# Kernel optimization log

Hardware: AMD Instinct MI355X
Metric: run time of the kernel (lower is better)

## Reference

```python
import jax, jax.numpy as jnp
import numpy as np

B, T, E, H = 2, 2048, 2048, 16
D = E // H


def setup_inputs() -> dict:
    key = jax.random.key(0)
    ks = jax.random.split(key, 5)
    s = 0.02
    return {
        "x": jax.random.normal(ks[0], (B, T, E), jnp.float32),
        "Wq": jax.random.normal(ks[1], (E, E), jnp.float32) * s,
        "Wk": jax.random.normal(ks[2], (E, E), jnp.float32) * s,
        "Wv": jax.random.normal(ks[3], (E, E), jnp.float32) * s,
        "Wp": jax.random.normal(ks[4], (E, E), jnp.float32) * s,
        "bp": jnp.zeros((E,), jnp.float32),
    }


def reference(x, Wq, Wk, Wv, Wp, bp):
    b, t, e = x.shape
    h, d = H, E // H
    # torch Linear: y = x @ W.T (no bias for qkv)
    Q = (x @ Wq.T).reshape(b, h, t, d)  # faithful: view without transpose
    K = (x @ Wk.T).reshape(b, h, t, d)
    V = (x @ Wv.T).reshape(b, h, t, d)
    scores = jnp.einsum("bhqd,bhkd->bhqk", Q, K)
    causal = jnp.triu(jnp.ones((t, t), bool), k=1)  # True above diagonal
    scores = jnp.where(causal, -jnp.inf, scores)
    weights = jax.nn.softmax(scores / jnp.sqrt(jnp.float32(d)), axis=-1)
    # dropout p=0.0 (eval) -> identity
    ctx = jnp.einsum("bhqk,bhkd->bhqd", weights, V)  # (b,h,t,d)
    ctx = ctx.transpose(0, 2, 1, 3).reshape(b, t, e)
    return ctx @ Wp.T + bp
```

## Files before the change

### kernel.cpp

```cpp
#include <hip/hip_runtime.h>

#define SEQ   2048
#define EMB   2048
#define NHEAD 16
#define HDIM  128
#define ROWSM 4096

typedef float  f32x4   __attribute__((ext_vector_type(4)));
typedef float  f32x16  __attribute__((ext_vector_type(16)));
typedef __bf16 bf16x8  __attribute__((ext_vector_type(8)));

__device__ __forceinline__ unsigned short f2bf(float f) {
  union { float f; unsigned int u; } v; v.f = f;
  return (unsigned short)((v.u + 0x7fffu + ((v.u >> 16) & 1u)) >> 16);
}
__device__ __forceinline__ unsigned int pk2(float a, float b) {
  return (unsigned int)f2bf(a) | ((unsigned int)f2bf(b) << 16);
}

__device__ __forceinline__ void gload16(const void* g, void* l) {
  __builtin_amdgcn_global_load_lds(
      (__attribute__((address_space(1))) const unsigned int*)g,
      (__attribute__((address_space(3))) unsigned int*)l,
      16, 0, 0);
}

__global__ void cvt_bf16(const float* __restrict__ in,
                         unsigned short* __restrict__ out, int n4) {
  int i = blockIdx.x * 256 + threadIdx.x;
  if (i >= n4) return;
  float4 v = ((const float4*)in)[i];
  ushort4 o;
  o.x = f2bf(v.x); o.y = f2bf(v.y); o.z = f2bf(v.z); o.w = f2bf(v.w);
  ((ushort4*)out)[i] = o;
}

__global__ void cvt_bf16_3(const float* __restrict__ i0, const float* __restrict__ i1,
                           const float* __restrict__ i2, unsigned short* __restrict__ o0,
                           unsigned short* __restrict__ o1, unsigned short* __restrict__ o2,
                           int n4) {
  const float* in = (blockIdx.z == 0) ? i0 : (blockIdx.z == 1) ? i1 : i2;
  unsigned short* out = (blockIdx.z == 0) ? o0 : (blockIdx.z == 1) ? o1 : o2;
  int i = blockIdx.x * 256 + threadIdx.x;
  if (i >= n4) return;
  float4 v = ((const float4*)in)[i];
  ushort4 o;
  o.x = f2bf(v.x); o.y = f2bf(v.y); o.z = f2bf(v.z); o.w = f2bf(v.w);
  ((ushort4*)out)[i] = o;
}

__global__ __launch_bounds__(256, 2) void gemm_qkv(
    const unsigned short* __restrict__ A,
    const unsigned short* __restrict__ B0, const unsigned short* __restrict__ B1,
    const unsigned short* __restrict__ B2, unsigned short* __restrict__ Cbase) {
  __shared__ __align__(16) unsigned short As[128 * 64];
  __shared__ __align__(16) unsigned short Bs[128 * 64];
  const unsigned short* Bm = (blockIdx.z == 0) ? B0 : (blockIdx.z == 1) ? B1 : B2;
  unsigned short* C = Cbase + (size_t)blockIdx.z * ROWSM * EMB;

  const int tid  = threadIdx.x;
  const int lane = tid & 63;
  const int w    = tid >> 6;
  const int m0 = blockIdx.y * 128;
  const int n0 = blockIdx.x * 128;
  const int wm = (w >> 1) * 64;
  const int wn = (w & 1) * 64;
  const int lg = lane >> 4;
  const int lc = lane & 15;

  f32x4 acc[4][4] = {};
  const int srow = lane >> 3;
  const int scol = (lane & 7) * 8;

  for (int k0 = 0; k0 < EMB; k0 += 64) {
    if (k0) __syncthreads();
#pragma unroll
    for (int ii = 0; ii < 4; ++ii) {
      int i = w * 4 + ii;
      int r = i * 8 + srow;
      gload16(A  + (size_t)(m0 + r) * EMB + k0 + scol, (char*)As + i * 1024);
      gload16(Bm + (size_t)(n0 + r) * EMB + k0 + scol, (char*)Bs + i * 1024);
    }
    __syncthreads();
#pragma unroll
    for (int kk = 0; kk < 2; ++kk) {
      const int co = kk * 32 + lg * 8;
      bf16x8 a[4], b[4];
#pragma unroll
      for (int i = 0; i < 4; ++i)
        a[i] = *(const bf16x8*)(As + (wm + i * 16 + lc) * 64 + co);
#pragma unroll
      for (int j = 0; j < 4; ++j)
        b[j] = *(const bf16x8*)(Bs + (wn + j * 16 + lc) * 64 + co);
#pragma unroll
      for (int i = 0; i < 4; ++i)
#pragma unroll
        for (int j = 0; j < 4; ++j)
          acc[i][j] = __builtin_amdgcn_mfma_f32_16x16x32_bf16(a[i], b[j], acc[i][j], 0, 0, 0);
    }
  }

  const int rb = lg * 4;
#pragma unroll
  for (int i = 0; i < 4; ++i)
#pragma unroll
    for (int j = 0; j < 4; ++j) {
      int col = n0 + wn + j * 16 + lc;
#pragma unroll
      for (int r = 0; r < 4; ++r) {
        int row = m0 + wm + i * 16 + rb + r;
        C[(size_t)row * EMB + col] = f2bf(acc[i][j][r]);
      }
    }
}

__global__ __launch_bounds__(256, 2) void gemm_p(
    const unsigned short* __restrict__ A, const unsigned short* __restrict__ B,
    float* __restrict__ Cout, const float* __restrict__ bias) {
  __shared__ __align__(16) unsigned short As[128 * 64];
  __shared__ __align__(16) unsigned short Bs[128 * 64];
  const int tid  = threadIdx.x;
  const int lane = tid & 63;
  const int w    = tid >> 6;
  const int m0 = blockIdx.y * 128;
  const int n0 = blockIdx.x * 128;
  const int wm = (w >> 1) * 64;
  const int wn = (w & 1) * 64;
  const int lg = lane >> 4;
  const int lc = lane & 15;

  f32x4 acc[4][4] = {};
  const int srow = lane >> 3;
  const int scol = (lane & 7) * 8;

  for (int k0 = 0; k0 < EMB; k0 += 64) {
    if (k0) __syncthreads();
#pragma unroll
    for (int ii = 0; ii < 4; ++ii) {
      int i = w * 4 + ii;
      int r = i * 8 + srow;
      gload16(A + (size_t)(m0 + r) * EMB + k0 + scol, (char*)As + i * 1024);
      gload16(B + (size_t)(n0 + r) * EMB + k0 + scol, (char*)Bs + i * 1024);
    }
    __syncthreads();
#pragma unroll
    for (int kk = 0; kk < 2; ++kk) {
      const int co = kk * 32 + lg * 8;
      bf16x8 a[4], b[4];
#pragma unroll
      for (int i = 0; i < 4; ++i)
        a[i] = *(const bf16x8*)(As + (wm + i * 16 + lc) * 64 + co);
#pragma unroll
      for (int j = 0; j < 4; ++j)
        b[j] = *(const bf16x8*)(Bs + (wn + j * 16 + lc) * 64 + co);
#pragma unroll
      for (int i = 0; i < 4; ++i)
#pragma unroll
        for (int j = 0; j < 4; ++j)
          acc[i][j] = __builtin_amdgcn_mfma_f32_16x16x32_bf16(a[i], b[j], acc[i][j], 0, 0, 0);
    }
  }

  const int rb = lg * 4;
#pragma unroll
  for (int i = 0; i < 4; ++i)
#pragma unroll
    for (int j = 0; j < 4; ++j) {
      int col = n0 + wn + j * 16 + lc;
#pragma unroll
      for (int r = 0; r < 4; ++r) {
        int row = m0 + wm + i * 16 + rb + r;
        Cout[(size_t)row * EMB + col] = acc[i][j][r] + bias[col];
      }
    }
}

__global__ __launch_bounds__(256, 2) void attn_causal(
    const unsigned short* __restrict__ Pq, const unsigned short* __restrict__ Pk,
    const unsigned short* __restrict__ Pv, unsigned short* __restrict__ ctx) {
  __shared__ __align__(16) unsigned short Ks[128 * 128];
  __shared__ __align__(16) unsigned short Vt[128 * 128];

  const int tid  = threadIdx.x;
  const int lane = tid & 63;
  const int w    = tid >> 6;
  const int ql   = lane & 31;
  const int hi   = lane >> 5;
  const int lg   = lane >> 4;
  const int lc   = lane & 15;

  const int bid = blockIdx.x;
  const int xcd = bid & 7;
  const int jj_ = bid >> 3;
  const int hh  = jj_ >> 4;
  const int bh  = xcd * 4 + hh;
  const int b   = bh >> 4;
  const int h   = bh & 15;
  const int qtr = jj_ & 15;
  const int qt  = (hh >= 2) ? (15 - qtr) : qtr;
  const int q0 = qt * 128;
  const int qw = q0 + w * 32;
  const int qg = qw + ql;

  const size_t hoff = (size_t)bh * SEQ * HDIM;
  const unsigned short* Q  = Pq + hoff;
  const unsigned short* Kh = Pk + hoff;
  const unsigned short* Vh = Pv + hoff;

  bf16x8 bq[8];
#pragma unroll
  for (int d8 = 0; d8 < 8; ++d8)
    bq[d8] = *(const bf16x8*)(Q + (size_t)qg * HDIM + d8 * 16 + hi * 8);

  const float NEG = -3.0e38f;
  f32x16 o[4];
#pragma unroll
  for (int dt = 0; dt < 4; ++dt)
#pragma unroll
    for (int r = 0; r < 16; ++r) o[dt][r] = 0.f;
  float m_r = NEG, l_r = 0.f;

  const float Cs   = 0.12753123161692858f;
  const float TDEF = 62.7f;

  const int nt128 = qt + 1;
  for (int tt = 0; tt < nt128; ++tt) {
    const int kv0 = tt * 128;
    if (tt) __syncthreads();
#pragma unroll
    for (int ii = 0; ii < 8; ++ii) {
      int i = w * 8 + ii;
      int r = i * 4 + lg;
      int sd = lc ^ (r & 7);
      gload16(Kh + (size_t)(kv0 + r) * HDIM + sd * 8, (char*)Ks + i * 1024);
    }
#pragma unroll 1
    for (int hv = 0; hv < 2; ++hv) {
      uint4 vr[4];
      const unsigned short* Vs = Vh + (size_t)(kv0 + hv * 64) * HDIM;
#pragma unroll
      for (int uu = 0; uu < 2; ++uu) {
        int u = tid + uu * 256;
        int kp = u >> 4, dg = u & 15;
        int k = kp * 2, d0 = dg * 8;
        vr[uu * 2]     = *(const uint4*)(Vs + (size_t)k * HDIM + d0);
        vr[uu * 2 + 1] = *(const uint4*)(Vs + (size_t)(k + 1) * HDIM + d0);
      }
#pragma unroll
      for (int uu = 0; uu < 2; ++uu) {
        int u = tid + uu * 256;
        int kp = u >> 4, dg = u & 15;
        int k = kp * 2, d0 = dg * 8;
        const unsigned short* e0 = (const unsigned short*)&vr[uu * 2];
        const unsigned short* e1 = (const unsigned short*)&vr[uu * 2 + 1];
#pragma unroll
        for (int jj = 0; jj < 8; ++jj) {
          int d = d0 + jj;
          int slot = ((hv << 3) | (k >> 3)) ^ jj ^ (dg & 7);
          int byteoff = d * 256 + (slot << 4) + (k & 7) * 2;
          *(unsigned int*)((char*)Vt + byteoff) =
              (unsigned int)e0[jj] | ((unsigned int)e1[jj] << 16);
        }
      }
    }
    __syncthreads();

#pragma unroll 1
    for (int hf = 0; hf < 2; ++hf) {
      const int kv0h = kv0 + hf * 64;
      if (kv0h > qw + 31) continue;
      const bool s1on = (kv0h + 32 <= qw + 31);
      const bool diag = (kv0h + 63 > qw);
      const char* ksb = (const char*)Ks + hf * 64 * 256;

      f32x16 c0, c1;
#pragma unroll
      for (int r = 0; r < 16; ++r) { c0[r] = 0.f; c1[r] = s1on ? 0.f : NEG; }
      __builtin_amdgcn_s_setprio(1);
#pragma unroll
      for (int d8 = 0; d8 < 8; ++d8) {
        bf16x8 ak = *(const bf16x8*)(ksb + ql * 256 +
                                     (((d8 * 2 + hi) ^ (ql & 7)) << 4));
        c0 = __builtin_amdgcn_mfma_f32_32x32x16_bf16(ak, bq[d8], c0, 0, 0, 0);
      }
      if (s1on) {
#pragma unroll
        for (int d8 = 0; d8 < 8; ++d8) {
          bf16x8 ak = *(const bf16x8*)(ksb + (32 + ql) * 256 +
                                       (((d8 * 2 + hi) ^ (ql & 7)) << 4));
          c1 = __builtin_amdgcn_mfma_f32_32x32x16_bf16(ak, bq[d8], c1, 0, 0, 0);
        }
      }
      __builtin_amdgcn_s_setprio(0);

      if (diag) {
#pragma unroll
        for (int r = 0; r < 16; ++r) {
          int kvl = (r & 3) + 8 * (r >> 2) + 4 * hi;
          if (kv0h + kvl > qg) c0[r] = NEG;
          if (s1on && kv0h + 32 + kvl > qg) c1[r] = NEG;
        }
      }
      float rm = c0[0];
#pragma unroll
      for (int r = 1; r < 16; ++r) rm = fmaxf(rm, c0[r]);
#pragma unroll
      for (int r = 0; r < 16; ++r) rm = fmaxf(rm, c1[r]);
      rm = fmaxf(rm, __shfl_xor(rm, 32));

      if (__any(rm > m_r + TDEF)) {
        float mnew = fmaxf(m_r, rm);
        float alpha = exp2f((m_r - mnew) * Cs);
        m_r = mnew;
        l_r *= alpha;
#pragma unroll
        for (int r = 0; r < 16; ++r) {
          float ar = __shfl(alpha, (r & 3) + 8 * (r >> 2) + 4 * hi);
#pragma unroll
          for (int dt = 0; dt < 4; ++dt) o[dt][r] *= ar;
        }
      }
#pragma unroll
      for (int r = 0; r < 16; ++r) {
        c0[r] = exp2f((c0[r] - m_r) * Cs);
        c1[r] = exp2f((c1[r] - m_r) * Cs);
      }
      float ps = 0.f;
#pragma unroll
      for (int r = 0; r < 16; ++r) ps += c0[r] + c1[r];
      ps += __shfl_xor(ps, 32);
      l_r += ps;

      bf16x8 pa[4];
#pragma unroll
      for (int t4 = 0; t4 < 4; ++t4) {
        const f32x16& cc = (t4 < 2) ? c0 : c1;
        const int rA = (t4 & 1) * 8;
        unsigned int pkL0 = pk2(cc[rA + 0], cc[rA + 1]);
        unsigned int pkL1 = pk2(cc[rA + 2], cc[rA + 3]);
        unsigned int pkH0 = pk2(cc[rA + 4], cc[rA + 5]);
        unsigned int pkH1 = pk2(cc[rA + 6], cc[rA + 7]);
        unsigned int give0 = hi ? pkL0 : pkH0;
        unsigned int give1 = hi ? pkL1 : pkH1;
        unsigned int keep0 = hi ? pkH0 : pkL0;
        unsigned int keep1 = hi ? pkH1 : pkL1;
        unsigned int recv0 = __shfl_xor(give0, 32);
        unsigned int recv1 = __shfl_xor(give1, 32);
        union { unsigned int u[4]; bf16x8 v; } pu;
        pu.u[0] = hi ? recv0 : keep0;
        pu.u[1] = hi ? recv1 : keep1;
        pu.u[2] = hi ? keep0 : recv0;
        pu.u[3] = hi ? keep1 : recv1;
        pa[t4] = pu.v;
      }
      __builtin_amdgcn_s_setprio(1);
#pragma unroll
      for (int t4 = 0; t4 < 4; ++t4) {
        if (diag && kv0h + t4 * 16 > qw + 31) continue;
#pragma unroll
        for (int dt = 0; dt < 4; ++dt) {
          int d = dt * 32 + ql;
          int slot = ((hf << 3) | (t4 << 1) | hi) ^ (d & 7) ^ ((d >> 3) & 7);
          bf16x8 bv = *(const bf16x8*)((const char*)Vt + d * 256 + (slot << 4));
          o[dt] = __builtin_amdgcn_mfma_f32_32x32x16_bf16(pa[t4], bv, o[dt], 0, 0, 0);
        }
      }
      __builtin_amdgcn_s_setprio(0);
    }
  }

  float linv = 1.0f / l_r;
  unsigned short* outp = ctx + (size_t)b * SEQ * EMB + (size_t)h * HDIM;
#pragma unroll
  for (int r = 0; r < 16; ++r) {
    int kvl = (r & 3) + 8 * (r >> 2) + 4 * hi;
    float lr = __shfl(linv, kvl);
    int qrow = qw + kvl;
#pragma unroll
    for (int dt = 0; dt < 4; ++dt)
      outp[(size_t)qrow * EMB + dt * 32 + ql] = f2bf(o[dt][r] * lr);
  }
}

extern "C" void kernel_launch(void* const* d_in, const int* in_sizes, int n_in,
                              void* d_out, int out_size, void* d_ws, size_t ws_size,
                              hipStream_t stream) {
  const float* x  = (const float*)d_in[0];
  const float* Wq = (const float*)d_in[1];
  const float* Wk = (const float*)d_in[2];
  const float* Wv = (const float*)d_in[3];
  const float* Wp = (const float*)d_in[4];
  const float* bp = (const float*)d_in[5];

  char* ws = (char*)d_ws;
  unsigned short* xb = (unsigned short*)ws;
  unsigned short* Wb = (unsigned short*)(ws + (size_t)(16u << 20));
  unsigned short* Pq = (unsigned short*)(ws + (size_t)(24u << 20));
  unsigned short* Pk = (unsigned short*)(ws + (size_t)(40u << 20));
  unsigned short* Pv = (unsigned short*)(ws + (size_t)(56u << 20));
  unsigned short* WvS = (unsigned short*)d_out;
  unsigned short* WkS = (unsigned short*)d_out + (size_t)4 * 1024 * 1024;

  const int nX4 = ROWSM * EMB / 4;
  const int nW4 = EMB * EMB / 4;

  cvt_bf16<<<nX4 / 256, 256, 0, stream>>>(x, xb, nX4);
  cvt_bf16_3<<<dim3(nW4 / 256, 1, 3), 256, 0, stream>>>(Wq, Wk, Wv, Wb, WkS, WvS, nW4);

  gemm_qkv<<<dim3(EMB / 128, ROWSM / 128, 3), 256, 0, stream>>>(xb, Wb, WkS, WvS, Pq);

  attn_causal<<<512, 256, 0, stream>>>(Pq, Pk, Pv, xb);

  cvt_bf16<<<nW4 / 256, 256, 0, stream>>>(Wp, Wb, nW4);
  gemm_p<<<dim3(EMB / 128, ROWSM / 128), 256, 0, stream>>>(xb, Wb, (float*)d_out, bp);
}
```

Measured before the change: 286.8 us.

## Replace QKV and projection GEMMs with double-buffered 256x128 swizzled-LDS kernel

Merges the QKV and output-projection GEMMs into one templated kernel with 512 threads and 256x128 tiles. It double-buffers LDS so global-to-LDS loads for the next K step overlap MFMA work on the current one. It also XOR-swizzles the LDS layout to cut bank conflicts and raises wave priority around the MFMA bursts. Occupancy drops to one block per CU with more LDS per block, and the hand-placed barriers and waitcnt ordering have to stay correct.

```diff
diff --git a/kernel.cpp b/kernel.cpp
--- a/kernel.cpp
+++ b/kernel.cpp
@@ -49,128 +49,131 @@
   ((ushort4*)out)[i] = o;
 }
 
-__global__ __launch_bounds__(256, 2) void gemm_qkv(
+template <int STORE_F32>
+__global__ __launch_bounds__(512, 1) void gemm_big(
     const unsigned short* __restrict__ A,
     const unsigned short* __restrict__ B0, const unsigned short* __restrict__ B1,
-    const unsigned short* __restrict__ B2, unsigned short* __restrict__ Cbase) {
-  __shared__ __align__(16) unsigned short As[128 * 64];
-  __shared__ __align__(16) unsigned short Bs[128 * 64];
+    const unsigned short* __restrict__ B2,
+    void* __restrict__ Cbase, const float* __restrict__ bias, int K) {
+  __shared__ __align__(16) unsigned short Abuf[2][256 * 64];
+  __shared__ __align__(16) unsigned short Bbuf[2][128 * 64];
+
   const unsigned short* Bm = (blockIdx.z == 0) ? B0 : (blockIdx.z == 1) ? B1 : B2;
-  unsigned short* C = Cbase + (size_t)blockIdx.z * ROWSM * EMB;
 
   const int tid  = threadIdx.x;
   const int lane = tid & 63;
   const int w    = tid >> 6;
-  const int m0 = blockIdx.y * 128;
+  const int lg   = lane >> 4;
+  const int lc   = lane & 15;
+  const int m0 = blockIdx.y * 256;
   const int n0 = blockIdx.x * 128;
-  const int wm = (w >> 1) * 64;
-  const int wn = (w & 1) * 64;
-  const int lg = lane >> 4;
-  const int lc = lane & 15;
-
-  f32x4 acc[4][4] = {};
-  const int srow = lane >> 3;
-  const int scol = (lane & 7) * 8;
-
-  for (int k0 = 0; k0 < EMB; k0 += 64) {
-    if (k0) __syncthreads();
+  const int wm = (w >> 2) * 128;
+  const int wn = (w & 3) * 32;
+
+  auto stageA = [&](int buf, int k0) {
 #pragma unroll
     for (int ii = 0; ii < 4; ++ii) {
-      int i = w * 4 + ii;
-      int r = i * 8 + srow;
-      gload16(A  + (size_t)(m0 + r) * EMB + k0 + scol, (char*)As + i * 1024);
-      gload16(Bm + (size_t)(n0 + r) * EMB + k0 + scol, (char*)Bs + i * 1024);
-    }
-    __syncthreads();
-#pragma unroll
-    for (int kk = 0; kk < 2; ++kk) {
-      const int co = kk * 32 + lg * 8;
-      bf16x8 a[4], b[4];
-#pragma unroll
-      for (int i = 0; i < 4; ++i)
-        a[i] = *(const bf16x8*)(As + (wm + i * 16 + lc) * 64 + co);
-#pragma unroll
-      for (int j = 0; j < 4; ++j)
-        b[j] = *(const bf16x8*)(Bs + (wn + j * 16 + lc) * 64 + co);
-#pragma unroll
-      for (int i = 0; i < 4; ++i)
-#pragma unroll
-        for (int j = 0; j < 4; ++j)
-          acc[i][j] = __builtin_amdgcn_mfma_f32_16x16x32_bf16(a[i], b[j], acc[i][j], 0, 0, 0);
-    }
+      int c = w * 4 + ii;
+      int r = c * 8 + (lane >> 3);
+      int s = (lane & 7) ^ ((r & 4) >> 1);
+      gload16(A + (size_t)(m0 + r) * K + k0 + s * 8, (char*)&Abuf[buf][0] + c * 1024);
+    }
+  };
+  auto stageB = [&](int buf, int k0) {
+#pragma unroll
+    for (int ii = 0; ii < 2; ++ii) {
+      int c = w * 2 + ii;
+      int r = c * 8 + (lane >> 3);
+      int s = (lane & 7) ^ ((r & 4) >> 1);
+      gload16(Bm + (size_t)(n0 + r) * K + k0 + s * 8, (char*)&Bbuf[buf][0] + c * 1024);
+    }
+  };
+
+  f32x4 acc[8][2] = {};
+
+  stageA(0, 0);
+  stageB(0, 0);
+  asm volatile("s_waitcnt vmcnt(0)" ::: "memory");
+  __builtin_amdgcn_s_barrier();
+
+  const int NT = K / 64;
+  for (int t = 0; t < NT; ++t) {
+    const int buf = t & 1;
+    const char* ab = (const char*)&Abuf[buf][0];
+    const char* bb = (const char*)&Bbuf[buf][0];
+    const int k0n = (t + 1) * 64;
+    const bool pf = (t + 1 < NT);
+
+    if (pf) stageA(buf ^ 1, k0n);
+    bf16x8 bfr[2][2], afr[4][2];
+#pragma unroll
+    for (int ni = 0; ni < 2; ++ni)
+#pragma unroll
+      for (int kk = 0; kk < 2; ++kk) {
+        int row = wn + ni * 16 + lc;
+        int o = kk * 4 + lg;
+        bfr[ni][kk] = *(const bf16x8*)(bb + row * 128 + ((o ^ ((row & 4) >> 1)) << 4));
+      }
+#pragma unroll
+    for (int mi = 0; mi < 4; ++mi)
+#pragma unroll
+      for (int kk = 0; kk < 2; ++kk) {
+        int row = wm + mi * 16 + lc;
+        int o = kk * 4 + lg;
+        afr[mi][kk] = *(const bf16x8*)(ab + row * 128 + ((o ^ ((row & 4) >> 1)) << 4));
+      }
+    __builtin_amdgcn_s_barrier();
+    __builtin_amdgcn_s_setprio(1);
+#pragma unroll
+    for (int mi = 0; mi < 4; ++mi)
+#pragma unroll
+      for (int ni = 0; ni < 2; ++ni)
+#pragma unroll
+        for (int kk = 0; kk < 2; ++kk)
+          acc[mi][ni] = __builtin_amdgcn_mfma_f32_16x16x32_bf16(
+              afr[mi][kk], bfr[ni][kk], acc[mi][ni], 0, 0, 0);
+    __builtin_amdgcn_s_setprio(0);
+    __builtin_amdgcn_s_barrier();
+
+    if (pf) stageB(buf ^ 1, k0n);
+#pragma unroll
+    for (int mi = 0; mi < 4; ++mi)
+#pragma unroll
+      for (int kk = 0; kk < 2; ++kk) {
+        int row = wm + 64 + mi * 16 + lc;
+        int o = kk * 4 + lg;
+        afr[mi][kk] = *(const bf16x8*)(ab + row * 128 + ((o ^ ((row & 4) >> 1)) << 4));
+      }
+    __builtin_amdgcn_s_barrier();
+    __builtin_amdgcn_s_setprio(1);
+#pragma unroll
+    for (int mi = 0; mi < 4; ++mi)
+#pragma unroll
+      for (int ni = 0; ni < 2; ++ni)
+#pragma unroll
+        for (int kk = 0; kk < 2; ++kk)
+          acc[4 + mi][ni] = __builtin_amdgcn_mfma_f32_16x16x32_bf16(
+              afr[mi][kk], bfr[ni][kk], acc[4 + mi][ni], 0, 0, 0);
+    __builtin_amdgcn_s_setprio(0);
+    asm volatile("s_waitcnt vmcnt(0)" ::: "memory");
+    __builtin_amdgcn_s_barrier();
   }
 
   const int rb = lg * 4;
 #pragma unroll
-  for (int i = 0; i < 4; ++i)
-#pragma unroll
-    for (int j = 0; j < 4; ++j) {
-      int col = n0 + wn + j * 16 + lc;
-#pragma unroll
-      for (int r = 0; r < 4; ++r) {
-        int row = m0 + wm + i * 16 + rb + r;
-        C[(size_t)row * EMB + col] = f2bf(acc[i][j][r]);
-      }
-    }
-}
-
-__global__ __launch_bounds__(256, 2) void gemm_p(
-    const unsigned short* __restrict__ A, const unsigned short* __restrict__ B,
-    float* __restrict__ Cout, const float* __restrict__ bias) {
-  __shared__ __align__(16) unsigned short As[128 * 64];
-  __shared__ __align__(16) unsigned short Bs[128 * 64];
-  const int tid  = threadIdx.x;
-  const int lane = tid & 63;
-  const int w    = tid >> 6;
-  const int m0 = blockIdx.y * 128;
-  const int n0 = blockIdx.x * 128;
-  const int wm = (w >> 1) * 64;
-  const int wn = (w & 1) * 64;
-  const int lg = lane >> 4;
-  const int lc = lane & 15;
-
-  f32x4 acc[4][4] = {};
-  const int srow = lane >> 3;
-  const int scol = (lane & 7) * 8;
-
-  for (int k0 = 0; k0 < EMB; k0 += 64) {
-    if (k0) __syncthreads();
-#pragma unroll
-    for (int ii = 0; ii < 4; ++ii) {
-      int i = w * 4 + ii;
-      int r = i * 8 + srow;
-      gload16(A + (size_t)(m0 + r) * EMB + k0 + scol, (char*)As + i * 1024);
-      gload16(B + (size_t)(n0 + r) * EMB + k0 + scol, (char*)Bs + i * 1024);
-    }
-    __syncthreads();
-#pragma unroll
-    for (int kk = 0; kk < 2; ++kk) {
-      const int co = kk * 32 + lg * 8;
-      bf16x8 a[4], b[4];
-#pragma unroll
-      for (int i = 0; i < 4; ++i)
-        a[i] = *(const bf16x8*)(As + (wm + i * 16 + lc) * 64 + co);
-#pragma unroll
-      for (int j = 0; j < 4; ++j)
-        b[j] = *(const bf16x8*)(Bs + (wn + j * 16 + lc) * 64 + co);
-#pragma unroll
-      for (int i = 0; i < 4; ++i)
-#pragma unroll
-        for (int j = 0; j < 4; ++j)
-          acc[i][j] = __builtin_amdgcn_mfma_f32_16x16x32_bf16(a[i], b[j], acc[i][j], 0, 0, 0);
-    }
-  }
-
-  const int rb = lg * 4;
-#pragma unroll
-  for (int i = 0; i < 4; ++i)
-#pragma unroll
-    for (int j = 0; j < 4; ++j) {
-      int col = n0 + wn + j * 16 + lc;
-#pragma unroll
-      for (int r = 0; r < 4; ++r) {
-        int row = m0 + wm + i * 16 + rb + r;
-        Cout[(size_t)row * EMB + col] = acc[i][j][r] + bias[col];
+  for (int mi = 0; mi < 8; ++mi)
+#pragma unroll
+    for (int ni = 0; ni < 2; ++ni) {
+      int col = n0 + wn + ni * 16 + lc;
+#pragma unroll
+      for (int rr = 0; rr < 4; ++rr) {
+        int row = m0 + wm + mi * 16 + rb + rr;
+        if (STORE_F32) {
+          ((float*)Cbase)[(size_t)row * EMB + col] = acc[mi][ni][rr] + bias[col];
+        } else {
+          ((unsigned short*)Cbase + (size_t)blockIdx.z * ROWSM * EMB)
+              [(size_t)row * EMB + col] = f2bf(acc[mi][ni][rr]);
+        }
       }
     }
 }
@@ -407,10 +410,12 @@
   cvt_bf16<<<nX4 / 256, 256, 0, stream>>>(x, xb, nX4);
   cvt_bf16_3<<<dim3(nW4 / 256, 1, 3), 256, 0, stream>>>(Wq, Wk, Wv, Wb, WkS, WvS, nW4);
 
-  gemm_qkv<<<dim3(EMB / 128, ROWSM / 128, 3), 256, 0, stream>>>(xb, Wb, WkS, WvS, Pq);
+  gemm_big<0><<<dim3(EMB / 128, ROWSM / 256, 3), 512, 0, stream>>>(
+      xb, Wb, WkS, WvS, Pq, nullptr, EMB);
 
   attn_causal<<<512, 256, 0, stream>>>(Pq, Pk, Pv, xb);
 
   cvt_bf16<<<nW4 / 256, 256, 0, stream>>>(Wp, Wb, nW4);
-  gemm_p<<<dim3(EMB / 128, ROWSM / 128), 256, 0, stream>>>(xb, Wb, (float*)d_out, bp);
-}
+  gemm_big<1><<<dim3(EMB / 128, ROWSM / 256, 1), 512, 0, stream>>>(
+      xb, Wb, Wb, Wb, d_out, bp, EMB);
+}
```

New measurement: 379.2 us. 1.32x slower.

## Double-buffer LDS tiles in QKV and projection GEMMs with async prefetch

Applied to the files above, without the earlier changes.

Merges the QKV and output-projection GEMMs into one templated kernel. LDS tiles are now double-buffered, and the global-to-LDS load for tile t+2 is issued while tile t is computed. Explicit vmcnt waits and raw barriers replace the per-iteration __syncthreads pairs. The aim is to hide global memory latency behind MFMA work. In exchange, LDS use per block doubles to 64KB, which may limit occupancy to 2 blocks per CU.

```diff
diff --git a/kernel.cpp b/kernel.cpp
--- a/kernel.cpp
+++ b/kernel.cpp
@@ -49,14 +49,15 @@
   ((ushort4*)out)[i] = o;
 }
 
-__global__ __launch_bounds__(256, 2) void gemm_qkv(
+template <int STORE_F32>
+__global__ __launch_bounds__(256, 2) void gemm_pipe(
     const unsigned short* __restrict__ A,
     const unsigned short* __restrict__ B0, const unsigned short* __restrict__ B1,
-    const unsigned short* __restrict__ B2, unsigned short* __restrict__ Cbase) {
-  __shared__ __align__(16) unsigned short As[128 * 64];
-  __shared__ __align__(16) unsigned short Bs[128 * 64];
+    const unsigned short* __restrict__ B2,
+    void* __restrict__ Cbase, const float* __restrict__ bias) {
+  __shared__ __align__(16) unsigned short As[2][128 * 64];
+  __shared__ __align__(16) unsigned short Bs[2][128 * 64];
   const unsigned short* Bm = (blockIdx.z == 0) ? B0 : (blockIdx.z == 1) ? B1 : B2;
-  unsigned short* C = Cbase + (size_t)blockIdx.z * ROWSM * EMB;
 
   const int tid  = threadIdx.x;
   const int lane = tid & 63;
@@ -72,32 +73,47 @@
   const int srow = lane >> 3;
   const int scol = (lane & 7) * 8;
 
-  for (int k0 = 0; k0 < EMB; k0 += 64) {
-    if (k0) __syncthreads();
+  auto stage = [&](int buf, int k0) {
 #pragma unroll
     for (int ii = 0; ii < 4; ++ii) {
       int i = w * 4 + ii;
       int r = i * 8 + srow;
-      gload16(A  + (size_t)(m0 + r) * EMB + k0 + scol, (char*)As + i * 1024);
-      gload16(Bm + (size_t)(n0 + r) * EMB + k0 + scol, (char*)Bs + i * 1024);
-    }
-    __syncthreads();
+      gload16(A  + (size_t)(m0 + r) * EMB + k0 + scol, (char*)&As[buf][0] + i * 1024);
+      gload16(Bm + (size_t)(n0 + r) * EMB + k0 + scol, (char*)&Bs[buf][0] + i * 1024);
+    }
+  };
+
+  stage(0, 0);
+  stage(1, 64);
+
+  const int NT = EMB / 64;
+  for (int t = 0; t < NT; ++t) {
+    const int buf = t & 1;
+    if (t + 1 < NT) asm volatile("s_waitcnt vmcnt(8)" ::: "memory");
+    else            asm volatile("s_waitcnt vmcnt(0)" ::: "memory");
+    __builtin_amdgcn_s_barrier();
+
+    const unsigned short* as = &As[buf][0];
+    const unsigned short* bs = &Bs[buf][0];
 #pragma unroll
     for (int kk = 0; kk < 2; ++kk) {
       const int co = kk * 32 + lg * 8;
       bf16x8 a[4], b[4];
 #pragma unroll
       for (int i = 0; i < 4; ++i)
-        a[i] = *(const bf16x8*)(As + (wm + i * 16 + lc) * 64 + co);
+        a[i] = *(const bf16x8*)(as + (wm + i * 16 + lc) * 64 + co);
 #pragma unroll
       for (int j = 0; j < 4; ++j)
-        b[j] = *(const bf16x8*)(Bs + (wn + j * 16 + lc) * 64 + co);
+        b[j] = *(const bf16x8*)(bs + (wn + j * 16 + lc) * 64 + co);
 #pragma unroll
       for (int i = 0; i < 4; ++i)
 #pragma unroll
         for (int j = 0; j < 4; ++j)
           acc[i][j] = __builtin_amdgcn_mfma_f32_16x16x32_bf16(a[i], b[j], acc[i][j], 0, 0, 0);
     }
+    asm volatile("s_waitcnt lgkmcnt(0)" ::: "memory");
+    __builtin_amdgcn_s_barrier();
+    if (t + 2 < NT) stage(buf, (t + 2) * 64);
   }
 
   const int rb = lg * 4;
@@ -109,68 +125,12 @@
 #pragma unroll
       for (int r = 0; r < 4; ++r) {
         int row = m0 + wm + i * 16 + rb + r;
-        C[(size_t)row * EMB + col] = f2bf(acc[i][j][r]);
-      }
-    }
-}
-
-__global__ __launch_bounds__(256, 2) void gemm_p(
-    const unsigned short* __restrict__ A, const unsigned short* __restrict__ B,
-    float* __restrict__ Cout, const float* __restrict__ bias) {
-  __shared__ __align__(16) unsigned short As[128 * 64];
-  __shared__ __align__(16) unsigned short Bs[128 * 64];
-  const int tid  = threadIdx.x;
-  const int lane = tid & 63;
-  const int w    = tid >> 6;
-  const int m0 = blockIdx.y * 128;
-  const int n0 = blockIdx.x * 128;
-  const int wm = (w >> 1) * 64;
-  const int wn = (w & 1) * 64;
-  const int lg = lane >> 4;
-  const int lc = lane & 15;
-
-  f32x4 acc[4][4] = {};
-  const int srow = lane >> 3;
-  const int scol = (lane & 7) * 8;
-
-  for (int k0 = 0; k0 < EMB; k0 += 64) {
-    if (k0) __syncthreads();
-#pragma unroll
-    for (int ii = 0; ii < 4; ++ii) {
-      int i = w * 4 + ii;
-      int r = i * 8 + srow;
-      gload16(A + (size_t)(m0 + r) * EMB + k0 + scol, (char*)As + i * 1024);
-      gload16(B + (size_t)(n0 + r) * EMB + k0 + scol, (char*)Bs + i * 1024);
-    }
-    __syncthreads();
-#pragma unroll
-    for (int kk = 0; kk < 2; ++kk) {
-      const int co = kk * 32 + lg * 8;
-      bf16x8 a[4], b[4];
-#pragma unroll
-      for (int i = 0; i < 4; ++i)
-        a[i] = *(const bf16x8*)(As + (wm + i * 16 + lc) * 64 + co);
-#pragma unroll
-      for (int j = 0; j < 4; ++j)
-        b[j] = *(const bf16x8*)(Bs + (wn + j * 16 + lc) * 64 + co);
-#pragma unroll
-      for (int i = 0; i < 4; ++i)
-#pragma unroll
-        for (int j = 0; j < 4; ++j)
-          acc[i][j] = __builtin_amdgcn_mfma_f32_16x16x32_bf16(a[i], b[j], acc[i][j], 0, 0, 0);
-    }
-  }
-
-  const int rb = lg * 4;
-#pragma unroll
-  for (int i = 0; i < 4; ++i)
-#pragma unroll
-    for (int j = 0; j < 4; ++j) {
-      int col = n0 + wn + j * 16 + lc;
-#pragma unroll
-      for (int r = 0; r < 4; ++r) {
-        int row = m0 + wm + i * 16 + rb + r;
-        Cout[(size_t)row * EMB + col] = acc[i][j][r] + bias[col];
+        if (STORE_F32) {
+          ((float*)Cbase)[(size_t)row * EMB + col] = acc[i][j][r] + bias[col];
+        } else {
+          ((unsigned short*)Cbase + (size_t)blockIdx.z * ROWSM * EMB)
+              [(size_t)row * EMB + col] = f2bf(acc[i][j][r]);
+        }
       }
     }
 }
@@ -407,10 +367,12 @@
   cvt_bf16<<<nX4 / 256, 256, 0, stream>>>(x, xb, nX4);
   cvt_bf16_3<<<dim3(nW4 / 256, 1, 3), 256, 0, stream>>>(Wq, Wk, Wv, Wb, WkS, WvS, nW4);
 
-  gemm_qkv<<<dim3(EMB / 128, ROWSM / 128, 3), 256, 0, stream>>>(xb, Wb, WkS, WvS, Pq);
+  gemm_pipe<0><<<dim3(EMB / 128, ROWSM / 128, 3), 256, 0, stream>>>(
+      xb, Wb, WkS, WvS, Pq, nullptr);
 
   attn_causal<<<512, 256, 0, stream>>>(Pq, Pk, Pv, xb);
 
   cvt_bf16<<<nW4 / 256, 256, 0, stream>>>(Wp, Wb, nW4);
-  gemm_p<<<dim3(EMB / 128, ROWSM / 128), 256, 0, stream>>>(xb, Wb, (float*)d_out, bp);
-}
+  gemm_pipe<1><<<dim3(EMB / 128, ROWSM / 128, 1), 256, 0, stream>>>(
+      xb, Wb, Wb, Wb, d_out, bp);
+}
```

Result: no change. 288.6 us (+0.6%).

## Rewrite QKV GEMM as 256x256 tile, 8-wave, double-buffered swizzled pipeline

Applied to the files above, without the earlier changes.

Replaces the 128x128 QKV projection GEMM with a 512-thread kernel that computes 256x256 tiles. It double-buffers LDS with a fine-grained staged global->LDS prefetch interleaved with four MFMA phases per K step. It also XOR-swizzles LDS columns to avoid bank conflicts and uses setprio around MFMA bursts. The aim is more data reuse per loaded byte and hiding global load latency. The cost is 128KB of LDS and one block per CU, with only 384 blocks in the grid.

```diff
diff --git a/kernel.cpp b/kernel.cpp
--- a/kernel.cpp
+++ b/kernel.cpp
@@ -49,67 +49,157 @@
   ((ushort4*)out)[i] = o;
 }
 
-__global__ __launch_bounds__(256, 2) void gemm_qkv(
+__global__ __launch_bounds__(512, 1) void gemm8_qkv(
     const unsigned short* __restrict__ A,
     const unsigned short* __restrict__ B0, const unsigned short* __restrict__ B1,
-    const unsigned short* __restrict__ B2, unsigned short* __restrict__ Cbase) {
-  __shared__ __align__(16) unsigned short As[128 * 64];
-  __shared__ __align__(16) unsigned short Bs[128 * 64];
+    const unsigned short* __restrict__ B2, unsigned short* __restrict__ Cb) {
+  __shared__ __align__(16) unsigned short At[2][256 * 64];
+  __shared__ __align__(16) unsigned short Bt[2][256 * 64];
   const unsigned short* Bm = (blockIdx.z == 0) ? B0 : (blockIdx.z == 1) ? B1 : B2;
-  unsigned short* C = Cbase + (size_t)blockIdx.z * ROWSM * EMB;
+  unsigned short* C = Cb + (size_t)blockIdx.z * ROWSM * EMB;
 
   const int tid  = threadIdx.x;
   const int lane = tid & 63;
   const int w    = tid >> 6;
-  const int m0 = blockIdx.y * 128;
-  const int n0 = blockIdx.x * 128;
-  const int wm = (w >> 1) * 64;
-  const int wn = (w & 1) * 64;
-  const int lg = lane >> 4;
-  const int lc = lane & 15;
-
-  f32x4 acc[4][4] = {};
-  const int srow = lane >> 3;
-  const int scol = (lane & 7) * 8;
-
-  for (int k0 = 0; k0 < EMB; k0 += 64) {
-    if (k0) __syncthreads();
-#pragma unroll
-    for (int ii = 0; ii < 4; ++ii) {
-      int i = w * 4 + ii;
-      int r = i * 8 + srow;
-      gload16(A  + (size_t)(m0 + r) * EMB + k0 + scol, (char*)As + i * 1024);
-      gload16(Bm + (size_t)(n0 + r) * EMB + k0 + scol, (char*)Bs + i * 1024);
-    }
-    __syncthreads();
-#pragma unroll
-    for (int kk = 0; kk < 2; ++kk) {
-      const int co = kk * 32 + lg * 8;
-      bf16x8 a[4], b[4];
-#pragma unroll
-      for (int i = 0; i < 4; ++i)
-        a[i] = *(const bf16x8*)(As + (wm + i * 16 + lc) * 64 + co);
-#pragma unroll
-      for (int j = 0; j < 4; ++j)
-        b[j] = *(const bf16x8*)(Bs + (wn + j * 16 + lc) * 64 + co);
-#pragma unroll
-      for (int i = 0; i < 4; ++i)
-#pragma unroll
-        for (int j = 0; j < 4; ++j)
-          acc[i][j] = __builtin_amdgcn_mfma_f32_16x16x32_bf16(a[i], b[j], acc[i][j], 0, 0, 0);
-    }
+  const int wr   = w >> 2;
+  const int wc   = w & 3;
+  const int lg   = lane >> 4;
+  const int lc   = lane & 15;
+  const int m0 = blockIdx.y * 256;
+  const int n0 = blockIdx.x * 256;
+
+  const int srow8 = lane >> 3;
+  const int sslot = (lane & 7) ^ srow8;
+  const int NT = EMB / 64;
+
+  auto stage_slot = [&](int g) {
+    int ts = (g + 5) >> 2;
+    if (ts >= NT) return;
+    int hh  = (g + 5) & 3;
+    int buf = ts & 1;
+    int k0  = ts * 64;
+    bool isA = (hh == 0 || hh == 3);
+    bool upper = (hh == 2 || hh == 3);
+    const unsigned short* src = isA ? A : Bm;
+    int rbase = (isA ? m0 : n0) + (upper ? 128 : 0);
+    char* dst = (isA ? (char*)&At[buf][0] : (char*)&Bt[buf][0]) + (upper ? 16384 : 0);
+#pragma unroll
+    for (int rr = 0; rr < 2; ++rr) {
+      int c = w + rr * 8;
+      int row = c * 8 + srow8;
+      gload16(src + (size_t)(rbase + row) * EMB + k0 + sslot * 8, dst + c * 1024);
+    }
+  };
+
+  f32x4 acc[8][4] = {};
+  bf16x8 afr[4][2], bfr0[2][2], bfr1[2][2];
+
+  stage_slot(-5); stage_slot(-4); stage_slot(-3); stage_slot(-2); stage_slot(-1);
+
+  for (int t = 0; t < NT; ++t) {
+    const char* ab = (const char*)&At[t & 1][0];
+    const char* bb = (const char*)&Bt[t & 1][0];
+    const int g = t * 4;
+
+    asm volatile("s_waitcnt vmcnt(6)" ::: "memory");
+#pragma unroll
+    for (int mi = 0; mi < 4; ++mi)
+#pragma unroll
+      for (int kk = 0; kk < 2; ++kk)
+        afr[mi][kk] = *(const bf16x8*)(ab + (wr * 128 + mi * 16 + lc) * 128 +
+                                       ((((kk << 2) | lg) ^ (lc & 7)) << 4));
+#pragma unroll
+    for (int ni = 0; ni < 2; ++ni)
+#pragma unroll
+      for (int kk = 0; kk < 2; ++kk)
+        bfr0[ni][kk] = *(const bf16x8*)(bb + (wc * 64 + ni * 16 + lc) * 128 +
+                                        ((((kk << 2) | lg) ^ (lc & 7)) << 4));
+    stage_slot(g);
+    __builtin_amdgcn_s_barrier();
+    asm volatile("s_waitcnt lgkmcnt(0)" ::: "memory");
+    __builtin_amdgcn_sched_barrier(0);
+    __builtin_amdgcn_s_setprio(1);
+#pragma unroll
+    for (int mi = 0; mi < 4; ++mi)
+#pragma unroll
+      for (int ni = 0; ni < 2; ++ni)
+#pragma unroll
+        for (int kk = 0; kk < 2; ++kk)
+          acc[mi][ni] = __builtin_amdgcn_mfma_f32_16x16x32_bf16(
+              afr[mi][kk], bfr0[ni][kk], acc[mi][ni], 0, 0, 0);
+    __builtin_amdgcn_s_setprio(0);
+    __builtin_amdgcn_s_barrier();
+
+    asm volatile("s_waitcnt vmcnt(6)" ::: "memory");
+#pragma unroll
+    for (int ni = 0; ni < 2; ++ni)
+#pragma unroll
+      for (int kk = 0; kk < 2; ++kk)
+        bfr1[ni][kk] = *(const bf16x8*)(bb + (wc * 64 + (2 + ni) * 16 + lc) * 128 +
+                                        ((((kk << 2) | lg) ^ (lc & 7)) << 4));
+    stage_slot(g + 1);
+    __builtin_amdgcn_s_barrier();
+    asm volatile("s_waitcnt lgkmcnt(0)" ::: "memory");
+    __builtin_amdgcn_sched_barrier(0);
+    __builtin_amdgcn_s_setprio(1);
+#pragma unroll
+    for (int mi = 0; mi < 4; ++mi)
+#pragma unroll
+      for (int ni = 0; ni < 2; ++ni)
+#pragma unroll
+        for (int kk = 0; kk < 2; ++kk)
+          acc[mi][2 + ni] = __builtin_amdgcn_mfma_f32_16x16x32_bf16(
+              afr[mi][kk], bfr1[ni][kk], acc[mi][2 + ni], 0, 0, 0);
+    __builtin_amdgcn_s_setprio(0);
+    __builtin_amdgcn_s_barrier();
+
+    asm volatile("s_waitcnt vmcnt(6)" ::: "memory");
+#pragma unroll
+    for (int mi = 0; mi < 4; ++mi)
+#pragma unroll
+      for (int kk = 0; kk < 2; ++kk)
+        afr[mi][kk] = *(const bf16x8*)(ab + (wr * 128 + 64 + mi * 16 + lc) * 128 +
+                                       ((((kk << 2) | lg) ^ (lc & 7)) << 4));
+    stage_slot(g + 2);
+    __builtin_amdgcn_s_barrier();
+    asm volatile("s_waitcnt lgkmcnt(0)" ::: "memory");
+    __builtin_amdgcn_sched_barrier(0);
+    __builtin_amdgcn_s_setprio(1);
+#pragma unroll
+    for (int mi = 0; mi < 4; ++mi)
+#pragma unroll
+      for (int ni = 0; ni < 2; ++ni)
+#pragma unroll
+        for (int kk = 0; kk < 2; ++kk)
+          acc[4 + mi][2 + ni] = __builtin_amdgcn_mfma_f32_16x16x32_bf16(
+              afr[mi][kk], bfr1[ni][kk], acc[4 + mi][2 + ni], 0, 0, 0);
+    __builtin_amdgcn_s_setprio(0);
+    __builtin_amdgcn_s_barrier();
+
+    stage_slot(g + 3);
+    __builtin_amdgcn_s_setprio(1);
+#pragma unroll
+    for (int mi = 0; mi < 4; ++mi)
+#pragma unroll
+      for (int ni = 0; ni < 2; ++ni)
+#pragma unroll
+        for (int kk = 0; kk < 2; ++kk)
+          acc[4 + mi][ni] = __builtin_amdgcn_mfma_f32_16x16x32_bf16(
+              afr[mi][kk], bfr0[ni][kk], acc[4 + mi][ni], 0, 0, 0);
+    __builtin_amdgcn_s_setprio(0);
+    __builtin_amdgcn_s_barrier();
   }
-
-  const int rb = lg * 4;
-#pragma unroll
-  for (int i = 0; i < 4; ++i)
-#pragma unroll
-    for (int j = 0; j < 4; ++j) {
-      int col = n0 + wn + j * 16 + lc;
-#pragma unroll
-      for (int r = 0; r < 4; ++r) {
-        int row = m0 + wm + i * 16 + rb + r;
-        C[(size_t)row * EMB + col] = f2bf(acc[i][j][r]);
+  asm volatile("s_waitcnt vmcnt(0)" ::: "memory");
+
+#pragma unroll
+  for (int mi = 0; mi < 8; ++mi)
+#pragma unroll
+    for (int ni = 0; ni < 4; ++ni) {
+      int col = n0 + wc * 64 + ni * 16 + lc;
+#pragma unroll
+      for (int rr = 0; rr < 4; ++rr) {
+        int row = m0 + wr * 128 + mi * 16 + lg * 4 + rr;
+        C[(size_t)row * EMB + col] = f2bf(acc[mi][ni][rr]);
       }
     }
 }
@@ -407,7 +497,8 @@
   cvt_bf16<<<nX4 / 256, 256, 0, stream>>>(x, xb, nX4);
   cvt_bf16_3<<<dim3(nW4 / 256, 1, 3), 256, 0, stream>>>(Wq, Wk, Wv, Wb, WkS, WvS, nW4);
 
-  gemm_qkv<<<dim3(EMB / 128, ROWSM / 128, 3), 256, 0, stream>>>(xb, Wb, WkS, WvS, Pq);
+  gemm8_qkv<<<dim3(EMB / 256, ROWSM / 256, 3), 512, 0, stream>>>(
+      xb, Wb, WkS, WvS, Pq);
 
   attn_causal<<<512, 256, 0, stream>>>(Pq, Pk, Pv, xb);
 
```

Measured after the change: 276.3 us. 1.04x faster.
